# Kernel optimization log

Hardware: AMD Instinct MI355X
Metric: run time of the kernel (lower is better)

The kernel has to match this reference:

```python
import jax, jax.numpy as jnp
import numpy as np

K1, K2 = 3, 3
DIL = 1
PAD = (DIL * (K1 - 1) // 2, DIL * (K2 - 1) // 2)


def _unfold(x, k1, k2, dilation, padding):
    # x: [B, C, H, W] -> patches [B, C, k1*k2, H*W], matching F.unfold ordering
    B, C, H, W = x.shape
    p0, p1 = padding
    xp = jnp.pad(x, ((0, 0), (0, 0), (p0, p0), (p1, p1)))
    cols = []
    for i in range(k1):  # small fixed loop over kernel taps
        for j in range(k2):
            cols.append(xp[:, :, i * dilation:i * dilation + H, j * dilation:j * dilation + W])
    patches = jnp.stack(cols, axis=2)  # [B, C, k1*k2, H, W]
    return patches.reshape(B, C, k1 * k2, H * W)


def setup_inputs() -> dict:
    key = jax.random.key(0)
    k1, k2, k3, k4 = jax.random.split(key, 4)
    B, Cin, Cout, H, W = 32, 128, 128, 32, 32
    x = jax.random.normal(k1, (B, Cin, H, W), dtype=jnp.float32)
    mask = jax.random.uniform(k2, (1, K1 * K2, H * W), dtype=jnp.float32)
    weight = jax.random.normal(k3, (Cout, Cin, K1, K2), dtype=jnp.float32) * 0.05
    bias = jax.random.normal(k4, (Cout,), dtype=jnp.float32) * 0.05
    return {"x": x, "mask": mask, "weight": weight, "bias": bias}


def reference(x, mask, weight, bias):
    B, Cin, H, W = x.shape
    Cout = weight.shape[0]
    KK = K1 * K2
    # unfold -> [B, Cin, KK, L]
    patches = _unfold(x, K1, K2, DIL, PAD)
    # per-patch mask multiply (mask broadcasts over B and Cin): mask [1, KK, L]
    patches = patches * mask[:, None, :, :]  # [B, Cin, KK, L]
    # dense matmul with flattened weight [Cout, Cin*KK]
    wm = weight.reshape(Cout, Cin * KK)
    out = jnp.einsum('ok,bkl->bol', wm, patches.reshape(B, Cin * KK, H * W))
    out = out + bias[None, :, None]
    return out.reshape(B, Cout, H, W)
```

## Files before the change

kernel.cpp:

```cpp
#include <hip/hip_runtime.h>
#include <hip/hip_fp16.h>

typedef _Float16 half8 __attribute__((ext_vector_type(8)));
typedef float f32x4 __attribute__((ext_vector_type(4)));

#define CIN   128
#define COUT  128
#define HH    32
#define WW    32
#define LTOT  1024
#define KKT   9
#define KDIM  1152

#define ABUF  32768
#define BOFF  65536
#define SMEM_BYTES 114688

__global__ void prep_w_kernel(const float* __restrict__ w, _Float16* __restrict__ wt) {
  int i = blockIdx.x * 256 + threadIdx.x;
  int o = i / KDIM;
  int r = i - o * KDIM;
  int kk = r >> 7, c = r & 127;
  wt[i] = (_Float16)w[(o * CIN + c) * KKT + kk];
}

__device__ __forceinline__ void gld16(const char* g, char* l) {
  __builtin_amdgcn_global_load_lds(
      (const __attribute__((address_space(1))) void*)g,
      (__attribute__((address_space(3))) void*)l, 16, 0, 0);
}

__global__ __launch_bounds__(256, 1)
void conv_mfma_kernel(const float* __restrict__ x,
                      const _Float16* __restrict__ wt,
                      const float* __restrict__ mask,
                      const float* __restrict__ bias,
                      float* __restrict__ out) {
  extern __shared__ char smem[];
  const int tid = threadIdx.x;
  int bid = blockIdx.x;
  bid = (bid & 7) * 32 + (bid >> 3);
  const int b  = bid >> 3;
  const int l0 = (bid & 7) << 7;
  const int h0 = (bid & 7) << 2;

  const int lane = tid & 63, wid = tid >> 6;
  const int lr = lane & 15, lg = lane >> 4;
  const int mw = (wid >> 1) << 6;
  const int nw = (wid & 1) << 6;

  float mv[9][4];
  {
    const float* mr = mask + l0 + nw + lr;
#pragma unroll
    for (int kk = 0; kk < 9; ++kk)
#pragma unroll
      for (int nj = 0; nj < 4; ++nj)
        mv[kk][nj] = mr[kk * LTOT + nj * 16];
  }

  const int wv = tid & 31, cg = tid >> 5;
  const float* xb = x + (size_t)b * CIN * LTOT;
  for (int p = 0; p < 2; ++p) {
    const int q = cg + p * 8;
    char* bdst = smem + BOFF + wv * 256 + ((q ^ (wv & 15)) << 4);
    float fr[6][8];
#pragma unroll
    for (int r = 0; r < 6; ++r) {
      const int hg = h0 - 1 + r;
      if ((unsigned)hg < (unsigned)HH) {
        const float* s = xb + (size_t)q * 8 * LTOT + hg * WW + wv;
#pragma unroll
        for (int j = 0; j < 8; ++j) fr[r][j] = s[(size_t)j * LTOT];
      }
    }
    asm volatile("s_waitcnt vmcnt(0)" ::: "memory");
#pragma unroll
    for (int r = 0; r < 6; ++r) {
      const int hg = h0 - 1 + r;
      half8 v = (half8){0, 0, 0, 0, 0, 0, 0, 0};
      if ((unsigned)hg < (unsigned)HH) {
#pragma unroll
        for (int j = 0; j < 8; ++j) v[j] = (_Float16)fr[r][j];
      }
      *(half8*)(bdst + r * 8192) = v;
    }
  }
#pragma unroll
  for (int kk = 0; kk < 9; ++kk)
#pragma unroll
    for (int nj = 0; nj < 4; ++nj)
      asm volatile("" : "+v"(mv[kk][nj]));

  const int t4 = tid >> 4, ch = tid & 15;
  const int cx = (ch ^ (t4 & 15)) << 4;
  int asrc[8];
#pragma unroll
  for (int r = 0; r < 8; ++r) asrc[r] = (r * 16 + t4) * 2304 + cx;
  const char* wtc = (const char*)wt;
  auto stageA = [&](int kk) {
    const char* s = wtc + kk * 256;
    char* d = smem + (kk & 1) * ABUF + tid * 16;
#pragma unroll
    for (int r = 0; r < 8; ++r) gld16(s + asrc[r], d + r * 4096);
  };
  stageA(0);
  stageA(1);
  asm volatile("s_waitcnt lgkmcnt(0)" ::: "memory");

  f32x4 acc[4][4];
#pragma unroll
  for (int mi = 0; mi < 4; ++mi)
#pragma unroll
    for (int nj = 0; nj < 4; ++nj)
      acc[mi][nj] = (f32x4){0.f, 0.f, 0.f, 0.f};

#pragma unroll
  for (int kk = 0; kk < 9; ++kk) {
    if (kk < 8) asm volatile("s_waitcnt vmcnt(8)" ::: "memory");
    else        asm volatile("s_waitcnt vmcnt(0)" ::: "memory");
    __builtin_amdgcn_s_barrier();

    const char* A = smem + (kk & 1) * ABUF;
    const int di = (kk * 11) >> 5;
    const int dj = kk - 3 * di;

    const char* Bp[4];
    int xk[4];
    _Float16 mh[4];
#pragma unroll
    for (int nj = 0; nj < 4; ++nj) {
      const int wb = ((nj & 1) << 4) + lr + dj - 1;
      const bool vld = (unsigned)wb < (unsigned)WW;
      const int wc = vld ? wb : 0;
      const int hrow = (nw >> 5) + (nj >> 1) + di;
      Bp[nj] = smem + BOFF + hrow * 8192 + wc * 256;
      xk[nj] = wc & 15;
      mh[nj] = (_Float16)(vld ? mv[kk][nj] : 0.f);
    }
    const char* A0 = A + (mw + lr) * 256;

#pragma unroll
    for (int ks = 0; ks < 4; ++ks) {
      const int q = ks * 4 + lg;
      half8 a0 = *(const half8*)(A0 +     0 + ((q ^ lr) << 4));
      half8 a1 = *(const half8*)(A0 +  4096 + ((q ^ lr) << 4));
      half8 a2 = *(const half8*)(A0 +  8192 + ((q ^ lr) << 4));
      half8 a3 = *(const half8*)(A0 + 12288 + ((q ^ lr) << 4));
      half8 b0 = *(const half8*)(Bp[0] + ((q ^ xk[0]) << 4)) * mh[0];
      half8 b1 = *(const half8*)(Bp[1] + ((q ^ xk[1]) << 4)) * mh[1];
      half8 b2 = *(const half8*)(Bp[2] + ((q ^ xk[2]) << 4)) * mh[2];
      half8 b3 = *(const half8*)(Bp[3] + ((q ^ xk[3]) << 4)) * mh[3];
      acc[0][0] = __builtin_amdgcn_mfma_f32_16x16x32_f16(a0, b0, acc[0][0], 0, 0, 0);
      acc[1][0] = __builtin_amdgcn_mfma_f32_16x16x32_f16(a1, b0, acc[1][0], 0, 0, 0);
      acc[2][0] = __builtin_amdgcn_mfma_f32_16x16x32_f16(a2, b0, acc[2][0], 0, 0, 0);
      acc[3][0] = __builtin_amdgcn_mfma_f32_16x16x32_f16(a3, b0, acc[3][0], 0, 0, 0);
      acc[0][1] = __builtin_amdgcn_mfma_f32_16x16x32_f16(a0, b1, acc[0][1], 0, 0, 0);
      acc[1][1] = __builtin_amdgcn_mfma_f32_16x16x32_f16(a1, b1, acc[1][1], 0, 0, 0);
      acc[2][1] = __builtin_amdgcn_mfma_f32_16x16x32_f16(a2, b1, acc[2][1], 0, 0, 0);
      acc[3][1] = __builtin_amdgcn_mfma_f32_16x16x32_f16(a3, b1, acc[3][1], 0, 0, 0);
      acc[0][2] = __builtin_amdgcn_mfma_f32_16x16x32_f16(a0, b2, acc[0][2], 0, 0, 0);
      acc[1][2] = __builtin_amdgcn_mfma_f32_16x16x32_f16(a1, b2, acc[1][2], 0, 0, 0);
      acc[2][2] = __builtin_amdgcn_mfma_f32_16x16x32_f16(a2, b2, acc[2][2], 0, 0, 0);
      acc[3][2] = __builtin_amdgcn_mfma_f32_16x16x32_f16(a3, b2, acc[3][2], 0, 0, 0);
      acc[0][3] = __builtin_amdgcn_mfma_f32_16x16x32_f16(a0, b3, acc[0][3], 0, 0, 0);
      acc[1][3] = __builtin_amdgcn_mfma_f32_16x16x32_f16(a1, b3, acc[1][3], 0, 0, 0);
      acc[2][3] = __builtin_amdgcn_mfma_f32_16x16x32_f16(a2, b3, acc[2][3], 0, 0, 0);
      acc[3][3] = __builtin_amdgcn_mfma_f32_16x16x32_f16(a3, b3, acc[3][3], 0, 0, 0);
    }

    asm volatile("s_waitcnt lgkmcnt(0)" ::: "memory");
    __builtin_amdgcn_s_barrier();
    if (kk <= 6) stageA(kk + 2);
  }

  float* outb = out + (size_t)b * COUT * LTOT + l0;
#pragma unroll
  for (int mi = 0; mi < 4; ++mi) {
#pragma unroll
    for (int rr = 0; rr < 4; ++rr) {
      const int o = mw + mi * 16 + lg * 4 + rr;
      const float bv = bias[o];
      float* orow = outb + (size_t)o * LTOT + nw + lr;
#pragma unroll
      for (int nj = 0; nj < 4; ++nj)
        orow[nj * 16] = acc[mi][nj][rr] + bv;
    }
  }
}

extern "C" void kernel_launch(void* const* d_in, const int* in_sizes, int n_in,
                              void* d_out, int out_size, void* d_ws, size_t ws_size,
                              hipStream_t stream) {
  const float* x    = (const float*)d_in[0];
  const float* mask = (const float*)d_in[1];
  const float* w    = (const float*)d_in[2];
  const float* bias = (const float*)d_in[3];
  float* out = (float*)d_out;
  _Float16* wt = (_Float16*)d_ws;

  (void)hipFuncSetAttribute(reinterpret_cast<const void*>(conv_mfma_kernel),
                            hipFuncAttributeMaxDynamicSharedMemorySize, SMEM_BYTES);

  prep_w_kernel<<<576, 256, 0, stream>>>(w, wt);
  conv_mfma_kernel<<<256, 256, SMEM_BYTES, stream>>>(x, wt, mask, bias, out);
}
```

Measured before the change: 25.99 us.

## Split K across two wave groups with 512-thread blocks and LDS reduction

Doubles the block to 512 threads and splits each kernel-tap's 128-channel reduction between two halves of the waves, which then combine partial accumulators through LDS before the epilogue. Staging of the input tile and weight tiles is redistributed across the larger thread count, and MFMA sections are wrapped in raised wave priority. The aim is more waves per CU to hide LDS and memory latency with only 256 blocks on the device. The cost is an extra LDS reduction pass and barrier. The launch bound of 2 blocks per CU cannot be met with ~112KB LDS per block.

Result: faster. 25.31 us (-2.6%).

```diff
diff --git a/kernel.cpp b/kernel.cpp
--- a/kernel.cpp
+++ b/kernel.cpp
@@ -30,7 +30,7 @@
       (__attribute__((address_space(3))) void*)l, 16, 0, 0);
 }
 
-__global__ __launch_bounds__(256, 1)
+__global__ __launch_bounds__(512, 2)
 void conv_mfma_kernel(const float* __restrict__ x,
                       const _Float16* __restrict__ wt,
                       const float* __restrict__ mask,
@@ -46,8 +46,10 @@
 
   const int lane = tid & 63, wid = tid >> 6;
   const int lr = lane & 15, lg = lane >> 4;
-  const int mw = (wid >> 1) << 6;
-  const int nw = (wid & 1) << 6;
+  const int kh = wid >> 2;
+  const int wq = wid & 3;
+  const int mw = (wq >> 1) << 6;
+  const int nw = (wq & 1) << 6;
 
   float mv[9][4];
   {
@@ -59,17 +61,16 @@
         mv[kk][nj] = mr[kk * LTOT + nj * 16];
   }
 
-  const int wv = tid & 31, cg = tid >> 5;
+  const int wv = tid & 31, q16 = tid >> 5;
+  char* bdst = smem + BOFF + wv * 256 + ((q16 ^ (wv & 15)) << 4);
   const float* xb = x + (size_t)b * CIN * LTOT;
-  for (int p = 0; p < 2; ++p) {
-    const int q = cg + p * 8;
-    char* bdst = smem + BOFF + wv * 256 + ((q ^ (wv & 15)) << 4);
+  {
     float fr[6][8];
 #pragma unroll
     for (int r = 0; r < 6; ++r) {
       const int hg = h0 - 1 + r;
       if ((unsigned)hg < (unsigned)HH) {
-        const float* s = xb + (size_t)q * 8 * LTOT + hg * WW + wv;
+        const float* s = xb + (size_t)q16 * 8 * LTOT + hg * WW + wv;
 #pragma unroll
         for (int j = 0; j < 8; ++j) fr[r][j] = s[(size_t)j * LTOT];
       }
@@ -94,15 +95,15 @@
 
   const int t4 = tid >> 4, ch = tid & 15;
   const int cx = (ch ^ (t4 & 15)) << 4;
-  int asrc[8];
-#pragma unroll
-  for (int r = 0; r < 8; ++r) asrc[r] = (r * 16 + t4) * 2304 + cx;
+  int asrc[4];
+#pragma unroll
+  for (int r = 0; r < 4; ++r) asrc[r] = (r * 32 + t4) * 2304 + cx;
   const char* wtc = (const char*)wt;
   auto stageA = [&](int kk) {
     const char* s = wtc + kk * 256;
     char* d = smem + (kk & 1) * ABUF + tid * 16;
 #pragma unroll
-    for (int r = 0; r < 8; ++r) gld16(s + asrc[r], d + r * 4096);
+    for (int r = 0; r < 4; ++r) gld16(s + asrc[r], d + r * 8192);
   };
   stageA(0);
   stageA(1);
@@ -117,7 +118,7 @@
 
 #pragma unroll
   for (int kk = 0; kk < 9; ++kk) {
-    if (kk < 8) asm volatile("s_waitcnt vmcnt(8)" ::: "memory");
+    if (kk < 8) asm volatile("s_waitcnt vmcnt(4)" ::: "memory");
     else        asm volatile("s_waitcnt vmcnt(0)" ::: "memory");
     __builtin_amdgcn_s_barrier();
 
@@ -140,9 +141,10 @@
     }
     const char* A0 = A + (mw + lr) * 256;
 
-#pragma unroll
-    for (int ks = 0; ks < 4; ++ks) {
-      const int q = ks * 4 + lg;
+    __builtin_amdgcn_s_setprio(1);
+#pragma unroll
+    for (int s = 0; s < 2; ++s) {
+      const int q = (kh * 2 + s) * 4 + lg;
       half8 a0 = *(const half8*)(A0 +     0 + ((q ^ lr) << 4));
       half8 a1 = *(const half8*)(A0 +  4096 + ((q ^ lr) << 4));
       half8 a2 = *(const half8*)(A0 +  8192 + ((q ^ lr) << 4));
@@ -168,23 +170,46 @@
       acc[2][3] = __builtin_amdgcn_mfma_f32_16x16x32_f16(a2, b3, acc[2][3], 0, 0, 0);
       acc[3][3] = __builtin_amdgcn_mfma_f32_16x16x32_f16(a3, b3, acc[3][3], 0, 0, 0);
     }
+    __builtin_amdgcn_s_setprio(0);
 
     asm volatile("s_waitcnt lgkmcnt(0)" ::: "memory");
     __builtin_amdgcn_s_barrier();
     if (kk <= 6) stageA(kk + 2);
   }
 
-  float* outb = out + (size_t)b * COUT * LTOT + l0;
-#pragma unroll
-  for (int mi = 0; mi < 4; ++mi) {
-#pragma unroll
-    for (int rr = 0; rr < 4; ++rr) {
-      const int o = mw + mi * 16 + lg * 4 + rr;
-      const float bv = bias[o];
-      float* orow = outb + (size_t)o * LTOT + nw + lr;
+  char* red = smem + wq * 17408 + lane * 272;
+  if (kh == 1) {
+#pragma unroll
+    for (int mi = 0; mi < 4; ++mi)
 #pragma unroll
       for (int nj = 0; nj < 4; ++nj)
-        orow[nj * 16] = acc[mi][nj][rr] + bv;
+        *(f32x4*)(red + (mi * 4 + nj) * 16) = acc[mi][nj];
+  }
+  asm volatile("s_waitcnt lgkmcnt(0)" ::: "memory");
+  __builtin_amdgcn_s_barrier();
+
+  if (kh == 0) {
+#pragma unroll
+    for (int mi = 0; mi < 4; ++mi)
+#pragma unroll
+      for (int nj = 0; nj < 4; ++nj) {
+        f32x4 p = *(const f32x4*)(red + (mi * 4 + nj) * 16);
+        acc[mi][nj].x += p.x; acc[mi][nj].y += p.y;
+        acc[mi][nj].z += p.z; acc[mi][nj].w += p.w;
+      }
+
+    float* outb = out + (size_t)b * COUT * LTOT + l0;
+#pragma unroll
+    for (int mi = 0; mi < 4; ++mi) {
+#pragma unroll
+      for (int rr = 0; rr < 4; ++rr) {
+        const int o = mw + mi * 16 + lg * 4 + rr;
+        const float bv = bias[o];
+        float* orow = outb + (size_t)o * LTOT + nw + lr;
+#pragma unroll
+        for (int nj = 0; nj < 4; ++nj)
+          orow[nj * 16] = acc[mi][nj][rr] + bv;
+      }
     }
   }
 }
@@ -203,5 +228,5 @@
                             hipFuncAttributeMaxDynamicSharedMemorySize, SMEM_BYTES);
 
   prep_w_kernel<<<576, 256, 0, stream>>>(w, wt);
-  conv_mfma_kernel<<<256, 256, SMEM_BYTES, stream>>>(x, wt, mask, bias, out);
-}
+  conv_mfma_kernel<<<256, 512, SMEM_BYTES, stream>>>(x, wt, mask, bias, out);
+}
```
